# Kernel tuning notes

Hardware: AMD Instinct MI355X
Metric: run time of the kernel (lower is better)

## Reference

```python
import jax, jax.numpy as jnp
import numpy as np

DIM = 1024
NUM_HEADS = 16
HEAD_DIM = DIM // NUM_HEADS

def setup_inputs() -> dict:
    key = jax.random.key(0)
    ks = jax.random.split(key, 5)
    s = 1.0 / np.sqrt(DIM)
    x = jax.random.normal(ks[0], (2, 2048, DIM), dtype=jnp.float32)
    W_qkv = jax.random.uniform(ks[1], (DIM, 3 * DIM), dtype=jnp.float32, minval=-s, maxval=s)
    b_qkv = jax.random.uniform(ks[2], (3 * DIM,), dtype=jnp.float32, minval=-s, maxval=s)
    W_out = jax.random.uniform(ks[3], (DIM, DIM), dtype=jnp.float32, minval=-s, maxval=s)
    b_out = jax.random.uniform(ks[4], (DIM,), dtype=jnp.float32, minval=-s, maxval=s)
    return {"x": x, "W_qkv": W_qkv, "b_qkv": b_qkv, "W_out": W_out, "b_out": b_out}

def reference(x, W_qkv, b_qkv, W_out, b_out):
    B, S, _ = x.shape
    qkv = x @ W_qkv + b_qkv                       # [B,S,3*dim]
    q, k, v = jnp.split(qkv, 3, axis=-1)
    # [B,S,dim] -> [B,H,S,hd]
    def to_heads(t):
        return t.reshape(B, S, NUM_HEADS, HEAD_DIM).transpose(0, 2, 1, 3)
    q, k, v = to_heads(q), to_heads(k), to_heads(v)
    scale = HEAD_DIM ** -0.5
    scores = jnp.einsum('bhqd,bhkd->bhqk', q, k) * scale
    attn = jax.nn.softmax(scores, axis=-1)
    out = jnp.einsum('bhqk,bhkd->bhqd', attn, v)  # [B,H,S,hd]
    out = out.transpose(0, 2, 1, 3).reshape(B, S, DIM)
    return out @ W_out + b_out
```

## Files before the change

### kernel.cpp

```cpp
#include <hip/hip_runtime.h>
#include <math.h>

#define DIMM    1024
#define NHEADS  16
#define HDIM    64
#define BATCH   2
#define SEQ     2048
#define ROWS    (BATCH*SEQ)

typedef _Float16 f16x8 __attribute__((ext_vector_type(8)));
typedef _Float16 f16x4 __attribute__((ext_vector_type(4)));
typedef float    f32x4 __attribute__((ext_vector_type(4)));

__device__ inline void gl_lds16(const void* g, void* l) {
    __builtin_amdgcn_global_load_lds(
        (const __attribute__((address_space(1))) void*)g,
        (__attribute__((address_space(3))) void*)l, 16, 0, 0);
}

__device__ void tcvt64(const float* __restrict__ in, _Float16* __restrict__ out,
                       int K, int N, int k0, int n0, float (*tile)[65], int t)
{
    {
        const int c4 = (t & 15) * 4;
        const int r  = t >> 4;
        #pragma unroll
        for (int i = 0; i < 4; i++) {
            const int rr = r + 16 * i;
            float4 v = *(const float4*)(in + (size_t)(k0 + rr) * N + n0 + c4);
            tile[rr][c4] = v.x; tile[rr][c4 + 1] = v.y;
            tile[rr][c4 + 2] = v.z; tile[rr][c4 + 3] = v.w;
        }
    }
    __syncthreads();
    #pragma unroll
    for (int i = 0; i < 2; i++) {
        const int seg = t + 256 * i;
        const int n   = seg >> 3;
        const int kc  = (seg & 7) * 8;
        f16x8 o;
        #pragma unroll
        for (int j = 0; j < 8; j++) o[j] = (_Float16)tile[kc + j][n];
        *(f16x8*)(out + (size_t)(n0 + n) * K + k0 + kc) = o;
    }
}

__global__ __launch_bounds__(256)
void prep_kernel(const float* __restrict__ x, const float* __restrict__ Wqkv,
                 const float* __restrict__ Wout, _Float16* __restrict__ xh,
                 _Float16* __restrict__ wqkvt, _Float16* __restrict__ woutt)
{
    __shared__ float tile[64][65];
    const int bx = blockIdx.x;
    const int t  = threadIdx.x;
    if (bx < 2048) {
        const int i = bx * 256 + t;
        const float4 a = *(const float4*)(x + (size_t)i * 8);
        const float4 b = *(const float4*)(x + (size_t)i * 8 + 4);
        f16x8 o;
        o[0] = (_Float16)a.x; o[1] = (_Float16)a.y; o[2] = (_Float16)a.z; o[3] = (_Float16)a.w;
        o[4] = (_Float16)b.x; o[5] = (_Float16)b.y; o[6] = (_Float16)b.z; o[7] = (_Float16)b.w;
        *(f16x8*)(xh + (size_t)i * 8) = o;
    } else if (bx < 2816) {
        const int id = bx - 2048;
        const int gx = id % 48, gy = id / 48;
        tcvt64(Wqkv, wqkvt, DIMM, 3 * DIMM, gy * 64, gx * 64, tile, t);
    } else {
        const int id = bx - 2816;
        const int gx = id & 15, gy = id >> 4;
        tcvt64(Wout, woutt, DIMM, DIMM, gy * 64, gx * 64, tile, t);
    }
}

template<int MODE>
__global__ __launch_bounds__(256)
void hgemm_bias_kernel(const _Float16* __restrict__ A, const _Float16* __restrict__ Bt,
                       const float* __restrict__ bias, void* __restrict__ Cout,
                       _Float16* __restrict__ vtg, int N, int K)
{
    __shared__ _Float16 As[128 * 32];
    __shared__ _Float16 Bs[128 * 32];

    const int t    = threadIdx.x;
    const int w    = t >> 6, lane = t & 63;
    const int quad = lane >> 4, l16 = lane & 15;
    const int wr   = w >> 1, wc = w & 1;
    const int row0 = blockIdx.y * 128, col0 = blockIdx.x * 128;

    f32x4 acc[4][4];
    #pragma unroll
    for (int i = 0; i < 4; i++)
        #pragma unroll
        for (int j = 0; j < 4; j++)
            #pragma unroll
            for (int r = 0; r < 4; r++) acc[i][j][r] = 0.f;

    const int p0 = w * 128 + lane;
    const int p1 = p0 + 64;
    const int rA0 = p0 >> 2, kq0 = (p0 & 3) ^ ((p0 >> 4) & 3);
    const int rA1 = p1 >> 2, kq1 = (p1 & 3) ^ ((p1 >> 4) & 3);

    const _Float16* gA0 = A  + (size_t)(row0 + rA0) * K + kq0 * 8;
    const _Float16* gA1 = A  + (size_t)(row0 + rA1) * K + kq1 * 8;
    const _Float16* gB0 = Bt + (size_t)(col0 + rA0) * K + kq0 * 8;
    const _Float16* gB1 = Bt + (size_t)(col0 + rA1) * K + kq1 * 8;
    _Float16* lA0 = As + p0 * 8;
    _Float16* lA1 = As + p1 * 8;
    _Float16* lB0 = Bs + p0 * 8;
    _Float16* lB1 = Bs + p1 * 8;

    const int sx    = quad ^ ((l16 >> 2) & 3);
    const int abase = ((wr * 64 + l16) * 4 + sx) * 8;
    const int bbase = ((wc * 64 + l16) * 4 + sx) * 8;

    const int niter = K >> 5;
    for (int it = 0; it < niter; it++) {
        __syncthreads();
        gl_lds16(gA0, lA0); gl_lds16(gA1, lA1);
        gl_lds16(gB0, lB0); gl_lds16(gB1, lB1);
        gA0 += 32; gA1 += 32; gB0 += 32; gB1 += 32;
        __syncthreads();

        f16x8 af[4], bf[4];
        #pragma unroll
        for (int i = 0; i < 4; i++) {
            af[i] = *(const f16x8*)(As + abase + i * 512);
            bf[i] = *(const f16x8*)(Bs + bbase + i * 512);
        }
        #pragma unroll
        for (int i = 0; i < 4; i++)
            #pragma unroll
            for (int j = 0; j < 4; j++)
                acc[i][j] = __builtin_amdgcn_mfma_f32_16x16x32_f16(af[i], bf[j], acc[i][j], 0, 0, 0);
    }

    const bool vblock = (MODE == 1) && (col0 >= 2 * DIMM);
    #pragma unroll
    for (int j = 0; j < 4; j++) {
        const int col = col0 + wc * 64 + j * 16 + l16;
        const float bv = bias[col];
        #pragma unroll
        for (int i = 0; i < 4; i++) {
            const int row = row0 + wr * 64 + i * 16 + quad * 4;
            if (vblock) {
                const int dg  = col - 2 * DIMM;
                const int h   = dg >> 6, dl = dg & 63;
                const int b   = row >> 11, key = row & (SEQ - 1);
                f16x4 o;
                #pragma unroll
                for (int r = 0; r < 4; r++) o[r] = (_Float16)(acc[i][j][r] + bv);
                *(f16x4*)(vtg + ((size_t)((b * NHEADS + h) * 64 + dl)) * SEQ + key) = o;
            } else {
                #pragma unroll
                for (int r = 0; r < 4; r++) {
                    const float v = acc[i][j][r] + bv;
                    if (MODE == 1)
                        ((_Float16*)Cout)[(size_t)(row + r) * N + col] = (_Float16)v;
                    else
                        ((float*)Cout)[(size_t)(row + r) * N + col] = v;
                }
            }
        }
    }
}

__global__ __launch_bounds__(256, 4)
void flash_attn_kernel(const _Float16* __restrict__ qkv,
                       const _Float16* __restrict__ vtg,
                       _Float16* __restrict__ out)
{
    const int qt = blockIdx.x;
    const int bh = blockIdx.y;
    const int b  = bh >> 4, h = bh & 15;
    const int t    = threadIdx.x;
    const int w    = t >> 6;
    const int lane = t & 63;
    const int quad = lane >> 4;
    const int l16  = lane & 15;
    const int sw   = l16 & 7;

    __shared__ __align__(16) _Float16 Ks [64 * 64];
    __shared__ __align__(16) _Float16 Vts[64 * 64];
    __shared__ __align__(16) _Float16 Ps [64 * 72];

    const int q0 = qt * 64;
    const size_t rstr = 3 * DIMM;
    const _Float16* qbase = qkv + (size_t)b * SEQ * rstr;

    f16x8 qf[4][2];
    #pragma unroll
    for (int qb = 0; qb < 4; qb++) {
        const _Float16* qrow = qbase + (size_t)(q0 + qb * 16 + l16) * rstr + h * HDIM;
        qf[qb][0] = *(const f16x8*)(qrow + quad * 8);
        qf[qb][1] = *(const f16x8*)(qrow + 32 + quad * 8);
    }

    f32x4 Oacc[4];
    #pragma unroll
    for (int i = 0; i < 4; i++) Oacc[i] = (f32x4){0.f, 0.f, 0.f, 0.f};
    float lrow[4] = {0.f, 0.f, 0.f, 0.f};

    const int seg0 = t, seg1 = t + 256;
    const int r0 = seg0 >> 3, lb0 = (seg0 & 7) ^ (r0 & 7);
    const int r1 = seg1 >> 3, lb1 = (seg1 & 7) ^ (r1 & 7);
    const _Float16* gK0 = qbase + (size_t)r0 * rstr + DIMM + h * HDIM + lb0 * 8;
    const _Float16* gK1 = qbase + (size_t)r1 * rstr + DIMM + h * HDIM + lb1 * 8;
    const _Float16* gV0 = vtg + ((size_t)bh * 64 + r0) * SEQ + lb0 * 8;
    const _Float16* gV1 = vtg + ((size_t)bh * 64 + r1) * SEQ + lb1 * 8;

    const int kAbase = (16 * w + l16) * 64;
    const int pAbase = (16 * w + l16) * 72;
    const float SCL  = 0.18033688f;

    #pragma unroll 1
    for (int k0 = 0; k0 < SEQ; k0 += 64) {
        __syncthreads();
        gl_lds16(gK0 + (size_t)k0 * rstr, Ks  + seg0 * 8);
        gl_lds16(gK1 + (size_t)k0 * rstr, Ks  + seg1 * 8);
        gl_lds16(gV0 + k0,                Vts + seg0 * 8);
        gl_lds16(gV1 + k0,                Vts + seg1 * 8);
        __syncthreads();

        f16x8 kf0 = *(const f16x8*)(Ks + kAbase + ((0 + quad) ^ sw) * 8);
        f16x8 kf1 = *(const f16x8*)(Ks + kAbase + ((4 + quad) ^ sw) * 8);
        #pragma unroll
        for (int qb = 0; qb < 4; qb++) {
            f32x4 s = (f32x4){0.f, 0.f, 0.f, 0.f};
            s = __builtin_amdgcn_mfma_f32_16x16x32_f16(kf0, qf[qb][0], s, 0, 0, 0);
            s = __builtin_amdgcn_mfma_f32_16x16x32_f16(kf1, qf[qb][1], s, 0, 0, 0);
            float p0 = exp2f(s[0] * SCL);
            float p1 = exp2f(s[1] * SCL);
            float p2 = exp2f(s[2] * SCL);
            float p3 = exp2f(s[3] * SCL);
            lrow[qb] += (p0 + p1) + (p2 + p3);
            f16x4 pk;
            pk[0] = (_Float16)p0; pk[1] = (_Float16)p1;
            pk[2] = (_Float16)p2; pk[3] = (_Float16)p3;
            *(f16x4*)(Ps + (qb * 16 + l16) * 72 + 16 * w + 4 * quad) = pk;
        }
        __syncthreads();

        f16x8 pf0 = *(const f16x8*)(Ps + pAbase + quad * 8);
        f16x8 pf1 = *(const f16x8*)(Ps + pAbase + 32 + quad * 8);
        #pragma unroll
        for (int db = 0; db < 4; db++) {
            const int vrow = db * 16 + l16;
            f16x8 vf0 = *(const f16x8*)(Vts + vrow * 64 + ((0 + quad) ^ sw) * 8);
            f16x8 vf1 = *(const f16x8*)(Vts + vrow * 64 + ((4 + quad) ^ sw) * 8);
            Oacc[db] = __builtin_amdgcn_mfma_f32_16x16x32_f16(pf0, vf0, Oacc[db], 0, 0, 0);
            Oacc[db] = __builtin_amdgcn_mfma_f32_16x16x32_f16(pf1, vf1, Oacc[db], 0, 0, 0);
        }
    }

    #pragma unroll
    for (int qb = 0; qb < 4; qb++) {
        lrow[qb] += __shfl_xor(lrow[qb], 16);
        lrow[qb] += __shfl_xor(lrow[qb], 32);
    }
    __syncthreads();
    float* lbuf = (float*)Ks;
    if (lane < 16) {
        #pragma unroll
        for (int qb = 0; qb < 4; qb++) lbuf[w * 64 + qb * 16 + lane] = lrow[qb];
    }
    __syncthreads();
    const int qloc = 16 * w + quad * 4;
    float lrec[4];
    #pragma unroll
    for (int r = 0; r < 4; r++) {
        const int q = qloc + r;
        lrec[r] = 1.f / (lbuf[q] + lbuf[64 + q] + lbuf[128 + q] + lbuf[192 + q]);
    }
    #pragma unroll
    for (int db = 0; db < 4; db++) {
        #pragma unroll
        for (int r = 0; r < 4; r++) {
            out[(size_t)(b * SEQ + q0 + qloc + r) * DIMM + h * HDIM + db * 16 + l16] =
                (_Float16)(Oacc[db][r] * lrec[r]);
        }
    }
}

extern "C" void kernel_launch(void* const* d_in, const int* in_sizes, int n_in,
                              void* d_out, int out_size, void* d_ws, size_t ws_size,
                              hipStream_t stream)
{
    const float* x    = (const float*)d_in[0];
    const float* Wqkv = (const float*)d_in[1];
    const float* bqkv = (const float*)d_in[2];
    const float* Wout = (const float*)d_in[3];
    const float* bout = (const float*)d_in[4];
    float* out = (float*)d_out;

    _Float16* qkvh  = (_Float16*)d_ws;
    _Float16* attnh = qkvh  + (size_t)ROWS * 3 * DIMM;
    _Float16* xh    = attnh + (size_t)ROWS * DIMM;
    _Float16* wqkvt = xh    + (size_t)ROWS * DIMM;
    _Float16* woutt = wqkvt + (size_t)3 * DIMM * DIMM;
    _Float16* vtg   = woutt + (size_t)DIMM * DIMM;

    prep_kernel<<<3072, 256, 0, stream>>>(x, Wqkv, Wout, xh, wqkvt, woutt);
    {
        dim3 grid(3 * DIMM / 128, ROWS / 128);
        hgemm_bias_kernel<1><<<grid, 256, 0, stream>>>(xh, wqkvt, bqkv, qkvh, vtg, 3 * DIMM, DIMM);
    }
    {
        dim3 grid(SEQ / 64, BATCH * NHEADS);
        flash_attn_kernel<<<grid, 256, 0, stream>>>(qkvh, vtg, attnh);
    }
    {
        dim3 grid(DIMM / 128, ROWS / 128);
        hgemm_bias_kernel<0><<<grid, 256, 0, stream>>>(attnh, woutt, bout, out, nullptr, DIMM, DIMM);
    }
}
```

Before: 214.5 us.

## Double-buffer LDS tiles in GEMM and flash attention to overlap loads with MFMA

Both the QKV/output GEMM and the flash-attention kernel now use two LDS buffers. The next K-slice (or K/V tile) is prefetched with global_load_lds while MFMAs run on the current buffer, which removes one of the two barriers per iteration. The barrier in the attention loop before the P·V product becomes an LDS-only wait, so it no longer stalls on the outstanding prefetch. Attention occupancy is lowered to 3 blocks per CU to fit the larger LDS footprint, and the softmax exp is rewritten as __expf with the plain scale.

```diff
diff --git a/kernel.cpp b/kernel.cpp
--- a/kernel.cpp
+++ b/kernel.cpp
@@ -16,6 +16,10 @@
     __builtin_amdgcn_global_load_lds(
         (const __attribute__((address_space(1))) void*)g,
         (__attribute__((address_space(3))) void*)l, 16, 0, 0);
+}
+
+__device__ inline void barrier_lds_only() {
+    __asm__ volatile("s_waitcnt lgkmcnt(0)\n\ts_barrier" ::: "memory");
 }
 
 __device__ void tcvt64(const float* __restrict__ in, _Float16* __restrict__ out,
@@ -78,8 +82,8 @@
                        const float* __restrict__ bias, void* __restrict__ Cout,
                        _Float16* __restrict__ vtg, int N, int K)
 {
-    __shared__ _Float16 As[128 * 32];
-    __shared__ _Float16 Bs[128 * 32];
+    __shared__ _Float16 As[2][128 * 32];
+    __shared__ _Float16 Bs[2][128 * 32];
 
     const int t    = threadIdx.x;
     const int w    = t >> 6, lane = t & 63;
@@ -104,28 +108,32 @@
     const _Float16* gA1 = A  + (size_t)(row0 + rA1) * K + kq1 * 8;
     const _Float16* gB0 = Bt + (size_t)(col0 + rA0) * K + kq0 * 8;
     const _Float16* gB1 = Bt + (size_t)(col0 + rA1) * K + kq1 * 8;
-    _Float16* lA0 = As + p0 * 8;
-    _Float16* lA1 = As + p1 * 8;
-    _Float16* lB0 = Bs + p0 * 8;
-    _Float16* lB1 = Bs + p1 * 8;
+    const int o0 = p0 * 8, o1 = p1 * 8;
 
     const int sx    = quad ^ ((l16 >> 2) & 3);
     const int abase = ((wr * 64 + l16) * 4 + sx) * 8;
     const int bbase = ((wc * 64 + l16) * 4 + sx) * 8;
 
+    gl_lds16(gA0, As[0] + o0); gl_lds16(gA1, As[0] + o1);
+    gl_lds16(gB0, Bs[0] + o0); gl_lds16(gB1, Bs[0] + o1);
+    gA0 += 32; gA1 += 32; gB0 += 32; gB1 += 32;
+
     const int niter = K >> 5;
+    #pragma unroll 1
     for (int it = 0; it < niter; it++) {
+        const int cur = it & 1;
         __syncthreads();
-        gl_lds16(gA0, lA0); gl_lds16(gA1, lA1);
-        gl_lds16(gB0, lB0); gl_lds16(gB1, lB1);
-        gA0 += 32; gA1 += 32; gB0 += 32; gB1 += 32;
-        __syncthreads();
+        if (it + 1 < niter) {
+            gl_lds16(gA0, As[cur ^ 1] + o0); gl_lds16(gA1, As[cur ^ 1] + o1);
+            gl_lds16(gB0, Bs[cur ^ 1] + o0); gl_lds16(gB1, Bs[cur ^ 1] + o1);
+            gA0 += 32; gA1 += 32; gB0 += 32; gB1 += 32;
+        }
 
         f16x8 af[4], bf[4];
         #pragma unroll
         for (int i = 0; i < 4; i++) {
-            af[i] = *(const f16x8*)(As + abase + i * 512);
-            bf[i] = *(const f16x8*)(Bs + bbase + i * 512);
+            af[i] = *(const f16x8*)(As[cur] + abase + i * 512);
+            bf[i] = *(const f16x8*)(Bs[cur] + bbase + i * 512);
         }
         #pragma unroll
         for (int i = 0; i < 4; i++)
@@ -164,7 +172,7 @@
     }
 }
 
-__global__ __launch_bounds__(256, 4)
+__global__ __launch_bounds__(256, 3)
 void flash_attn_kernel(const _Float16* __restrict__ qkv,
                        const _Float16* __restrict__ vtg,
                        _Float16* __restrict__ out)
@@ -179,9 +187,10 @@
     const int l16  = lane & 15;
     const int sw   = l16 & 7;
 
-    __shared__ __align__(16) _Float16 Ks [64 * 64];
-    __shared__ __align__(16) _Float16 Vts[64 * 64];
-    __shared__ __align__(16) _Float16 Ps [64 * 72];
+    __shared__ __align__(16) _Float16 Kbuf[2][4096];
+    __shared__ __align__(16) _Float16 Vbuf[2][4096];
+    __shared__ __align__(16) _Float16 Ps[64 * 72];
+    __shared__ float lbuf[256];
 
     const int q0 = qt * 64;
     const size_t rstr = 3 * DIMM;
@@ -210,16 +219,25 @@
 
     const int kAbase = (16 * w + l16) * 64;
     const int pAbase = (16 * w + l16) * 72;
-    const float SCL  = 0.18033688f;
+
+    gl_lds16(gK0, Kbuf[0] + seg0 * 8);
+    gl_lds16(gK1, Kbuf[0] + seg1 * 8);
+    gl_lds16(gV0, Vbuf[0] + seg0 * 8);
+    gl_lds16(gV1, Vbuf[0] + seg1 * 8);
 
     #pragma unroll 1
-    for (int k0 = 0; k0 < SEQ; k0 += 64) {
+    for (int it = 0; it < SEQ / 64; it++) {
+        const int cur = it & 1;
         __syncthreads();
-        gl_lds16(gK0 + (size_t)k0 * rstr, Ks  + seg0 * 8);
-        gl_lds16(gK1 + (size_t)k0 * rstr, Ks  + seg1 * 8);
-        gl_lds16(gV0 + k0,                Vts + seg0 * 8);
-        gl_lds16(gV1 + k0,                Vts + seg1 * 8);
-        __syncthreads();
+        if (it + 1 < SEQ / 64) {
+            const size_t ko = (size_t)(it + 1) * 64;
+            gl_lds16(gK0 + ko * rstr, Kbuf[cur ^ 1] + seg0 * 8);
+            gl_lds16(gK1 + ko * rstr, Kbuf[cur ^ 1] + seg1 * 8);
+            gl_lds16(gV0 + ko,        Vbuf[cur ^ 1] + seg0 * 8);
+            gl_lds16(gV1 + ko,        Vbuf[cur ^ 1] + seg1 * 8);
+        }
+        const _Float16* Ks  = Kbuf[cur];
+        const _Float16* Vts = Vbuf[cur];
 
         f16x8 kf0 = *(const f16x8*)(Ks + kAbase + ((0 + quad) ^ sw) * 8);
         f16x8 kf1 = *(const f16x8*)(Ks + kAbase + ((4 + quad) ^ sw) * 8);
@@ -228,17 +246,17 @@
             f32x4 s = (f32x4){0.f, 0.f, 0.f, 0.f};
             s = __builtin_amdgcn_mfma_f32_16x16x32_f16(kf0, qf[qb][0], s, 0, 0, 0);
             s = __builtin_amdgcn_mfma_f32_16x16x32_f16(kf1, qf[qb][1], s, 0, 0, 0);
-            float p0 = exp2f(s[0] * SCL);
-            float p1 = exp2f(s[1] * SCL);
-            float p2 = exp2f(s[2] * SCL);
-            float p3 = exp2f(s[3] * SCL);
+            float p0 = __expf(s[0] * 0.125f);
+            float p1 = __expf(s[1] * 0.125f);
+            float p2 = __expf(s[2] * 0.125f);
+            float p3 = __expf(s[3] * 0.125f);
             lrow[qb] += (p0 + p1) + (p2 + p3);
             f16x4 pk;
             pk[0] = (_Float16)p0; pk[1] = (_Float16)p1;
             pk[2] = (_Float16)p2; pk[3] = (_Float16)p3;
             *(f16x4*)(Ps + (qb * 16 + l16) * 72 + 16 * w + 4 * quad) = pk;
         }
-        __syncthreads();
+        barrier_lds_only();
 
         f16x8 pf0 = *(const f16x8*)(Ps + pAbase + quad * 8);
         f16x8 pf1 = *(const f16x8*)(Ps + pAbase + 32 + quad * 8);
@@ -257,8 +275,6 @@
         lrow[qb] += __shfl_xor(lrow[qb], 16);
         lrow[qb] += __shfl_xor(lrow[qb], 32);
     }
-    __syncthreads();
-    float* lbuf = (float*)Ks;
     if (lane < 16) {
         #pragma unroll
         for (int qb = 0; qb < 4; qb++) lbuf[w * 64 + qb * 16 + lane] = lrow[qb];
```

Measured after the change: 211.2 us. Within noise of the previous version (-1.5%).
